# Optimization experiments

Hardware: AMD Instinct MI355X
Metric: run time of the kernel (lower is better)

Reference implementation:

```python
import jax, jax.numpy as jnp
import numpy as np

F8_MAX = 448.0  # max representable value of float8_e4m3fn


def setup_inputs() -> dict:
    key = jax.random.key(0)
    k1, k2, k3 = jax.random.split(key, 3)
    inp = jax.random.normal(k1, (4, 2048, 4096), dtype=jnp.float32)
    weight = jax.random.normal(k2, (4096, 16384), dtype=jnp.float32) * 0.02  # [in, out] (stored transposed)
    bias = jax.random.normal(k3, (16384,), dtype=jnp.float32)
    return {"inp": inp, "weight": weight, "bias": bias}


def reference(inp, weight, bias):
    # --- weight quantization (from_float with abs-max observer) ---
    w_scale = jnp.max(jnp.abs(weight)) / F8_MAX                      # scalar fp32
    w_q = (weight * (1.0 / w_scale)).astype(jnp.float8_e4m3fn)       # [in, out] fp8

    # --- dynamic input quantization: amax = max(|min|, |max|) ---
    x = inp.reshape(-1, inp.shape[-1])                               # [N, in]
    amax = jnp.maximum(jnp.abs(jnp.min(x)), jnp.abs(jnp.max(x)))
    x_scale = amax / F8_MAX
    x_q = (x * (1.0 / x_scale)).astype(jnp.float8_e4m3fn)            # [N, in] fp8

    # --- fp8_gemm_v2: dequant-matmul with fused scales + bias ---
    out = jnp.matmul(x_q.astype(jnp.float32), w_q.astype(jnp.float32))
    out = out * (x_scale * w_scale) + bias                           # [N, out]
    return out.reshape(inp.shape[:-1] + (weight.shape[1],))
```

## Files before the change

### kernel.cpp

```cpp
#include <hip/hip_runtime.h>
#include <stdint.h>
#include <stddef.h>

typedef float f32x16 __attribute__((ext_vector_type(16)));
typedef int i32x8 __attribute__((ext_vector_type(8)));

union Frag32 { long l[4]; i32x8 v; };


__global__ void absmax_kernel(const float4* __restrict__ x, size_t n4,
                              unsigned int* __restrict__ out) {
  size_t idx = (size_t)blockIdx.x * blockDim.x + threadIdx.x;
  size_t stride = (size_t)gridDim.x * blockDim.x;
  float m = 0.f;
  for (size_t i = idx; i < n4; i += stride) {
    float4 v = x[i];
    m = fmaxf(m, fmaxf(fmaxf(fabsf(v.x), fabsf(v.y)),
                       fmaxf(fabsf(v.z), fabsf(v.w))));
  }
#pragma unroll
  for (int off = 32; off > 0; off >>= 1)
    m = fmaxf(m, __shfl_xor(m, off));
  if ((threadIdx.x & 63) == 0)
    atomicMax(out, __float_as_uint(m));
}

__global__ void scales_kernel(float* __restrict__ s) {
  const unsigned int* u = (const unsigned int*)s;
  float wmax = __uint_as_float(u[0]);
  float xmax = __uint_as_float(u[1]);
  float w_scale = wmax / 448.0f;
  float x_scale = xmax / 448.0f;
  s[2] = 1.0f / w_scale;
  s[3] = 1.0f / x_scale;
  s[4] = x_scale * w_scale;
}

__global__ void quantize_x_kernel(const float4* __restrict__ x,
                                  uint8_t* __restrict__ xq,
                                  const float* __restrict__ scales,
                                  int K, int n_chunks) {
  const float inv = scales[3];
  const int kslots = K >> 5;
  int idx = blockIdx.x * blockDim.x + threadIdx.x;
  const int stride = gridDim.x * blockDim.x;
  for (; idx < n_chunks; idx += stride) {
    const int slot = idx >> 9;
    const int p16 = idx & 511;
    const int row = p16 >> 1;
    const int kkb0 = (p16 & 1) << 4;
    const int mblk = slot / kslots;
    const int ksl = slot - mblk * kslots;
    const size_t f4 = ((size_t)(mblk * 256 + row) * K + ksl * 32 + kkb0) >> 2;
    const float4 v0 = x[f4 + 0], v1 = x[f4 + 1], v2 = x[f4 + 2], v3 = x[f4 + 3];
    uint32_t c0 = __builtin_amdgcn_cvt_pk_fp8_f32(v0.x * inv, v0.y * inv, 0, false);
    c0 = __builtin_amdgcn_cvt_pk_fp8_f32(v0.z * inv, v0.w * inv, c0, true);
    uint32_t c1 = __builtin_amdgcn_cvt_pk_fp8_f32(v1.x * inv, v1.y * inv, 0, false);
    c1 = __builtin_amdgcn_cvt_pk_fp8_f32(v1.z * inv, v1.w * inv, c1, true);
    uint32_t c2 = __builtin_amdgcn_cvt_pk_fp8_f32(v2.x * inv, v2.y * inv, 0, false);
    c2 = __builtin_amdgcn_cvt_pk_fp8_f32(v2.z * inv, v2.w * inv, c2, true);
    uint32_t c3 = __builtin_amdgcn_cvt_pk_fp8_f32(v3.x * inv, v3.y * inv, 0, false);
    c3 = __builtin_amdgcn_cvt_pk_fp8_f32(v3.z * inv, v3.w * inv, c3, true);
    const unsigned long long L0 = (unsigned long long)c0 | ((unsigned long long)c1 << 32);
    const unsigned long long L1 = (unsigned long long)c2 | ((unsigned long long)c3 << 32);
    const int Lc = row * 32 + kkb0;
    const int mask = ((row >> 2) & 3) << 3;
    const int addr0 = Lc ^ (mask & 16);
    uint8_t* p = xq + (size_t)slot * 8192;
    *(unsigned long long*)(p + addr0 + (mask & 8)) = L0;
    *(unsigned long long*)(p + addr0 + (8 ^ (mask & 8))) = L1;
  }
}

__global__ void quantize_wT_kernel(const float* __restrict__ w,
                                   uint8_t* __restrict__ wqt,
                                   const float* __restrict__ scales,
                                   int N, int K) {
  __shared__ uint8_t tile[64][68];
  const float inv = scales[2];
  const int tn = blockIdx.x;
  const int tk = blockIdx.y;
  const int t = threadIdx.x;
  {
    const int rr = t >> 4;
    const int cc4 = t & 15;
#pragma unroll
    for (int i = 0; i < 4; ++i) {
      const int row = rr + i * 16;
      const float4 v = *(const float4*)&w[(size_t)(tk * 64 + row) * N + tn * 64 + cc4 * 4];
      uint32_t c = __builtin_amdgcn_cvt_pk_fp8_f32(v.x * inv, v.y * inv, 0, false);
      c = __builtin_amdgcn_cvt_pk_fp8_f32(v.z * inv, v.w * inv, c, true);
      *(uint32_t*)&tile[row][cc4 * 4] = c;
    }
  }
  __syncthreads();
  {
    const int nrow = t & 63;
    const int kc16 = t >> 6;
    unsigned long long L0 = 0, L1 = 0;
#pragma unroll
    for (int j = 0; j < 8; ++j)
      L0 |= (unsigned long long)tile[kc16 * 16 + j][nrow] << (8 * j);
#pragma unroll
    for (int j = 0; j < 8; ++j)
      L1 |= (unsigned long long)tile[kc16 * 16 + 8 + j][nrow] << (8 * j);
    const int n_g = tn * 64 + nrow;
    const int k0g = tk * 64 + kc16 * 16;
    const size_t slot = (size_t)(n_g >> 8) * (K >> 5) + (k0g >> 5);
    const int row = n_g & 255;
    const int kkb0 = k0g & 31;
    const int Lc = row * 32 + kkb0;
    const int mask = ((row >> 2) & 3) << 3;
    const int addr0 = Lc ^ (mask & 16);
    uint8_t* p = wqt + slot * 8192;
    *(unsigned long long*)(p + addr0 + (mask & 8)) = L0;
    *(unsigned long long*)(p + addr0 + (8 ^ (mask & 8))) = L1;
  }
}

#define T_BM 256
#define T_BN 256
#define UNIT_SCALE 0x7F7F7F7F

__device__ __forceinline__ void gl_lds16(const uint8_t* g, uint8_t* lds) {
  __builtin_amdgcn_global_load_lds(
      (const __attribute__((address_space(1))) void*)g,
      (__attribute__((address_space(3))) void*)lds, 16, 0, 0);
}

__global__ __launch_bounds__(1024, 4) void gemm_fp8_mx(
    const uint8_t* __restrict__ Aq, const uint8_t* __restrict__ BqT,
    const float* __restrict__ bias, const float* __restrict__ scales,
    float* __restrict__ C, int M, int N, int K) {
  extern __shared__ uint8_t smem[];
  uint8_t* const Ar = smem;
  uint8_t* const Br = smem + 65536;

  const int ntn = N / T_BN;
  const int bid = blockIdx.x;
  const int m0 = (bid / ntn) * T_BM;
  const int n0 = (bid % ntn) * T_BN;

  const int tid = threadIdx.x;
  const int w = tid >> 6;
  const int l = tid & 63;
  const int wr = w >> 2;
  const int wc = w & 3;

  const int kslots = K >> 5;

  const int soff = w * 1024 + l * 16;
  const uint8_t* a_src = Aq + (size_t)(m0 >> 8) * kslots * 8192 + soff;
  const uint8_t* b_src = BqT + (size_t)(n0 >> 8) * kslots * 8192 + soff;

  const int h = l >> 5;
  const int rl = l & 31;
  int aoff[2][4], boff[2][4];
#pragma unroll
  for (int mt = 0; mt < 2; ++mt) {
    const int ra = wr * 64 + mt * 32 + rl;
    const int rb = wc * 64 + mt * 32 + rl;
#pragma unroll
    for (int j = 0; j < 4; ++j) {
      aoff[mt][j] = h * 8192 + ra * 32 + ((j ^ ((ra >> 2) & 3)) * 8);
      boff[mt][j] = h * 8192 + rb * 32 + ((j ^ ((rb >> 2) & 3)) * 8);
    }
  }

  f32x16 acc[2][2];
#pragma unroll
  for (int i = 0; i < 2; ++i)
#pragma unroll
    for (int j = 0; j < 2; ++j) acc[i][j] = 0.f;

  const int NP = K >> 6;

  gl_lds16(a_src, Ar + soff);
  gl_lds16(b_src, Br + soff);
  gl_lds16(a_src + 16384, Ar + 16384 + soff);
  gl_lds16(b_src + 16384, Br + 16384 + soff);
  asm volatile("s_waitcnt vmcnt(2)" ::: "memory");
  __builtin_amdgcn_s_barrier();

  for (int p = 0; p < NP; ++p) {
    const int ss = (p + 2 < NP) ? (p + 2) : (p - 2);
    const int rslot = ((p + 2) & 3) * 16384;
    gl_lds16(a_src + (size_t)ss * 16384, Ar + rslot + soff);
    gl_lds16(b_src + (size_t)ss * 16384, Br + rslot + soff);

    const uint8_t* Asl = Ar + (p & 3) * 16384;
    const uint8_t* Bsl = Br + (p & 3) * 16384;
    Frag32 af[2], bf[2];
#pragma unroll
    for (int t2 = 0; t2 < 2; ++t2)
#pragma unroll
      for (int j = 0; j < 4; ++j) {
        af[t2].l[j] = *(const long*)(Asl + aoff[t2][j]);
        bf[t2].l[j] = *(const long*)(Bsl + boff[t2][j]);
      }

    __builtin_amdgcn_s_setprio(1);
    acc[0][0] = __builtin_amdgcn_mfma_scale_f32_32x32x64_f8f6f4(
        af[0].v, bf[0].v, acc[0][0], 0, 0, 0, UNIT_SCALE, 0, UNIT_SCALE);
    acc[1][0] = __builtin_amdgcn_mfma_scale_f32_32x32x64_f8f6f4(
        af[1].v, bf[0].v, acc[1][0], 0, 0, 0, UNIT_SCALE, 0, UNIT_SCALE);
    acc[0][1] = __builtin_amdgcn_mfma_scale_f32_32x32x64_f8f6f4(
        af[0].v, bf[1].v, acc[0][1], 0, 0, 0, UNIT_SCALE, 0, UNIT_SCALE);
    acc[1][1] = __builtin_amdgcn_mfma_scale_f32_32x32x64_f8f6f4(
        af[1].v, bf[1].v, acc[1][1], 0, 0, 0, UNIT_SCALE, 0, UNIT_SCALE);
    __builtin_amdgcn_s_setprio(0);

    asm volatile("s_waitcnt vmcnt(2)" ::: "memory");
    __builtin_amdgcn_s_barrier();
  }
  asm volatile("s_waitcnt vmcnt(0)" ::: "memory");

  const float s = scales[4];
  const int colb = n0 + wc * 64 + rl;
  const int rowb = m0 + wr * 64 + 4 * h;
#pragma unroll
  for (int nt = 0; nt < 2; ++nt) {
    const int col = colb + nt * 32;
    const float bv = bias[col];
#pragma unroll
    for (int mt = 0; mt < 2; ++mt) {
#pragma unroll
      for (int r = 0; r < 16; ++r) {
        const int row = rowb + mt * 32 + (r & 3) + 8 * (r >> 2);
        C[(size_t)row * N + col] = acc[mt][nt][r] * s + bv;
      }
    }
  }
}

extern "C" void kernel_launch(void* const* d_in, const int* in_sizes, int n_in,
                              void* d_out, int out_size, void* d_ws, size_t ws_size,
                              hipStream_t stream) {
  const float* inp = (const float*)d_in[0];
  const float* weight = (const float*)d_in[1];
  const float* bias = (const float*)d_in[2];
  float* out = (float*)d_out;

  const int N = in_sizes[2];
  const int K = in_sizes[1] / N;
  const int M = in_sizes[0] / K;

  uint8_t* ws = (uint8_t*)d_ws;
  float* scales = (float*)ws;
  uint8_t* xq = ws + 256;
  uint8_t* wqt = ws + 256 + (size_t)M * K;

  hipMemsetAsync(d_ws, 0, 256, stream);

  absmax_kernel<<<2048, 256, 0, stream>>>((const float4*)weight,
                                          (size_t)K * N / 4,
                                          (unsigned int*)ws + 0);
  absmax_kernel<<<2048, 256, 0, stream>>>((const float4*)inp,
                                          (size_t)M * K / 4,
                                          (unsigned int*)ws + 1);
  scales_kernel<<<1, 1, 0, stream>>>(scales);

  quantize_x_kernel<<<4096, 256, 0, stream>>>((const float4*)inp, xq, scales,
                                              K, M * K / 16);
  quantize_wT_kernel<<<dim3(N / 64, K / 64), 256, 0, stream>>>(weight, wqt,
                                                               scales, N, K);

  gemm_fp8_mx<<<(M / T_BM) * (N / T_BN), 1024, 131072, stream>>>(
      xq, wqt, bias, scales, out, M, N, K);
}
```

Before: 886.8 us.

## Enlarge per-wave GEMM tiles, rework weight transpose-quantize, drop scales kernel

The GEMM drops from 16 waves to 8 waves per block, and each wave now computes a 64x128 output tile with 8 MFMA accumulators instead of 4. This raises register-level reuse of A fragments and halves LDS fragment traffic per MFMA. The weight quantize kernel now transposes fp32 values through LDS, converts 32 consecutive k values per thread, and writes 16-byte stores instead of gathering bytes. The separate scales kernel is removed and each consumer computes its scale from the amax words, and absmax processes two float4 per iteration. The risks are higher register pressure and lower occupancy in the GEMM, plus a larger LDS tile in the transpose kernel.

```diff
diff --git a/kernel.cpp b/kernel.cpp
--- a/kernel.cpp
+++ b/kernel.cpp
@@ -10,14 +10,18 @@
 
 __global__ void absmax_kernel(const float4* __restrict__ x, size_t n4,
                               unsigned int* __restrict__ out) {
-  size_t idx = (size_t)blockIdx.x * blockDim.x + threadIdx.x;
-  size_t stride = (size_t)gridDim.x * blockDim.x;
-  float m = 0.f;
+  size_t idx = ((size_t)blockIdx.x * blockDim.x + threadIdx.x) * 2;
+  size_t stride = (size_t)gridDim.x * blockDim.x * 2;
+  float m0 = 0.f, m1 = 0.f;
   for (size_t i = idx; i < n4; i += stride) {
     float4 v = x[i];
-    m = fmaxf(m, fmaxf(fmaxf(fabsf(v.x), fabsf(v.y)),
-                       fmaxf(fabsf(v.z), fabsf(v.w))));
-  }
+    float4 u = x[i + 1];
+    m0 = fmaxf(m0, fmaxf(fmaxf(fabsf(v.x), fabsf(v.y)),
+                         fmaxf(fabsf(v.z), fabsf(v.w))));
+    m1 = fmaxf(m1, fmaxf(fmaxf(fabsf(u.x), fabsf(u.y)),
+                         fmaxf(fabsf(u.z), fabsf(u.w))));
+  }
+  float m = fmaxf(m0, m1);
 #pragma unroll
   for (int off = 32; off > 0; off >>= 1)
     m = fmaxf(m, __shfl_xor(m, off));
@@ -25,22 +29,12 @@
     atomicMax(out, __float_as_uint(m));
 }
 
-__global__ void scales_kernel(float* __restrict__ s) {
-  const unsigned int* u = (const unsigned int*)s;
-  float wmax = __uint_as_float(u[0]);
-  float xmax = __uint_as_float(u[1]);
-  float w_scale = wmax / 448.0f;
-  float x_scale = xmax / 448.0f;
-  s[2] = 1.0f / w_scale;
-  s[3] = 1.0f / x_scale;
-  s[4] = x_scale * w_scale;
-}
-
 __global__ void quantize_x_kernel(const float4* __restrict__ x,
                                   uint8_t* __restrict__ xq,
-                                  const float* __restrict__ scales,
+                                  const unsigned int* __restrict__ amax,
                                   int K, int n_chunks) {
-  const float inv = scales[3];
+  const float x_scale = __uint_as_float(amax[1]) / 448.0f;
+  const float inv = 1.0f / x_scale;
   const int kslots = K >> 5;
   int idx = blockIdx.x * blockDim.x + threadIdx.x;
   const int stride = gridDim.x * blockDim.x;
@@ -74,47 +68,54 @@
 
 __global__ void quantize_wT_kernel(const float* __restrict__ w,
                                    uint8_t* __restrict__ wqt,
-                                   const float* __restrict__ scales,
+                                   const unsigned int* __restrict__ amax,
                                    int N, int K) {
-  __shared__ uint8_t tile[64][68];
-  const float inv = scales[2];
+  __shared__ float tileF[64][129];
+  const float w_scale = __uint_as_float(amax[0]) / 448.0f;
+  const float inv = 1.0f / w_scale;
   const int tn = blockIdx.x;
   const int tk = blockIdx.y;
   const int t = threadIdx.x;
   {
-    const int rr = t >> 4;
-    const int cc4 = t & 15;
-#pragma unroll
-    for (int i = 0; i < 4; ++i) {
-      const int row = rr + i * 16;
-      const float4 v = *(const float4*)&w[(size_t)(tk * 64 + row) * N + tn * 64 + cc4 * 4];
-      uint32_t c = __builtin_amdgcn_cvt_pk_fp8_f32(v.x * inv, v.y * inv, 0, false);
-      c = __builtin_amdgcn_cvt_pk_fp8_f32(v.z * inv, v.w * inv, c, true);
-      *(uint32_t*)&tile[row][cc4 * 4] = c;
+    const int nn4 = t & 15;
+    const int kk0 = t >> 4;
+#pragma unroll
+    for (int i = 0; i < 8; ++i) {
+      const int kk = kk0 + i * 16;
+      const float4 v =
+          *(const float4*)&w[(size_t)(tk * 128 + kk) * N + tn * 64 + nn4 * 4];
+      tileF[nn4 * 4 + 0][kk] = v.x;
+      tileF[nn4 * 4 + 1][kk] = v.y;
+      tileF[nn4 * 4 + 2][kk] = v.z;
+      tileF[nn4 * 4 + 3][kk] = v.w;
     }
   }
   __syncthreads();
   {
-    const int nrow = t & 63;
-    const int kc16 = t >> 6;
-    unsigned long long L0 = 0, L1 = 0;
-#pragma unroll
-    for (int j = 0; j < 8; ++j)
-      L0 |= (unsigned long long)tile[kc16 * 16 + j][nrow] << (8 * j);
-#pragma unroll
-    for (int j = 0; j < 8; ++j)
-      L1 |= (unsigned long long)tile[kc16 * 16 + 8 + j][nrow] << (8 * j);
-    const int n_g = tn * 64 + nrow;
-    const int k0g = tk * 64 + kc16 * 16;
+    const int n = t & 63;
+    const int c = t >> 6;
+    unsigned long long q[4];
+#pragma unroll
+    for (int cc = 0; cc < 4; ++cc) {
+      const float4 u0 = *(const float4*)&tileF[n][c * 32 + cc * 8];
+      const float4 u1 = *(const float4*)&tileF[n][c * 32 + cc * 8 + 4];
+      uint32_t lo = __builtin_amdgcn_cvt_pk_fp8_f32(u0.x * inv, u0.y * inv, 0, false);
+      lo = __builtin_amdgcn_cvt_pk_fp8_f32(u0.z * inv, u0.w * inv, lo, true);
+      uint32_t hi = __builtin_amdgcn_cvt_pk_fp8_f32(u1.x * inv, u1.y * inv, 0, false);
+      hi = __builtin_amdgcn_cvt_pk_fp8_f32(u1.z * inv, u1.w * inv, hi, true);
+      q[cc] = (unsigned long long)lo | ((unsigned long long)hi << 32);
+    }
+    const int n_g = tn * 64 + n;
+    const int k0g = tk * 128 + c * 32;
     const size_t slot = (size_t)(n_g >> 8) * (K >> 5) + (k0g >> 5);
     const int row = n_g & 255;
-    const int kkb0 = k0g & 31;
-    const int Lc = row * 32 + kkb0;
-    const int mask = ((row >> 2) & 3) << 3;
-    const int addr0 = Lc ^ (mask & 16);
-    uint8_t* p = wqt + slot * 8192;
-    *(unsigned long long*)(p + addr0 + (mask & 8)) = L0;
-    *(unsigned long long*)(p + addr0 + (8 ^ (mask & 8))) = L1;
+    const int mask = (row >> 2) & 3;
+    ulonglong2 s0, s1;
+    s0.x = q[0 ^ mask]; s0.y = q[1 ^ mask];
+    s1.x = q[2 ^ mask]; s1.y = q[3 ^ mask];
+    uint8_t* pbase = wqt + slot * 8192 + row * 32;
+    *(ulonglong2*)(pbase) = s0;
+    *(ulonglong2*)(pbase + 16) = s1;
   }
 }
 
@@ -128,9 +129,9 @@
       (__attribute__((address_space(3))) void*)lds, 16, 0, 0);
 }
 
-__global__ __launch_bounds__(1024, 4) void gemm_fp8_mx(
+__global__ __launch_bounds__(512, 2) void gemm_fp8_mx(
     const uint8_t* __restrict__ Aq, const uint8_t* __restrict__ BqT,
-    const float* __restrict__ bias, const float* __restrict__ scales,
+    const float* __restrict__ bias, const unsigned int* __restrict__ amax,
     float* __restrict__ C, int M, int N, int K) {
   extern __shared__ uint8_t smem[];
   uint8_t* const Ar = smem;
@@ -144,82 +145,95 @@
   const int tid = threadIdx.x;
   const int w = tid >> 6;
   const int l = tid & 63;
-  const int wr = w >> 2;
-  const int wc = w & 3;
+  const int wr = w >> 1;
+  const int wc = w & 1;
 
   const int kslots = K >> 5;
 
-  const int soff = w * 1024 + l * 16;
+  const int soff = w * 2048 + l * 16;
   const uint8_t* a_src = Aq + (size_t)(m0 >> 8) * kslots * 8192 + soff;
   const uint8_t* b_src = BqT + (size_t)(n0 >> 8) * kslots * 8192 + soff;
 
   const int h = l >> 5;
   const int rl = l & 31;
-  int aoff[2][4], boff[2][4];
+  int aoff[2][4], boff[4][4];
 #pragma unroll
   for (int mt = 0; mt < 2; ++mt) {
     const int ra = wr * 64 + mt * 32 + rl;
-    const int rb = wc * 64 + mt * 32 + rl;
-#pragma unroll
-    for (int j = 0; j < 4; ++j) {
+#pragma unroll
+    for (int j = 0; j < 4; ++j)
       aoff[mt][j] = h * 8192 + ra * 32 + ((j ^ ((ra >> 2) & 3)) * 8);
-      boff[mt][j] = h * 8192 + rb * 32 + ((j ^ ((rb >> 2) & 3)) * 8);
-    }
-  }
-
-  f32x16 acc[2][2];
+  }
+#pragma unroll
+  for (int nt = 0; nt < 4; ++nt) {
+    const int rb = wc * 128 + nt * 32 + rl;
+#pragma unroll
+    for (int j = 0; j < 4; ++j)
+      boff[nt][j] = h * 8192 + rb * 32 + ((j ^ ((rb >> 2) & 3)) * 8);
+  }
+
+  f32x16 acc[2][4];
 #pragma unroll
   for (int i = 0; i < 2; ++i)
 #pragma unroll
-    for (int j = 0; j < 2; ++j) acc[i][j] = 0.f;
+    for (int j = 0; j < 4; ++j) acc[i][j] = 0.f;
 
   const int NP = K >> 6;
 
-  gl_lds16(a_src, Ar + soff);
-  gl_lds16(b_src, Br + soff);
-  gl_lds16(a_src + 16384, Ar + 16384 + soff);
-  gl_lds16(b_src + 16384, Br + 16384 + soff);
-  asm volatile("s_waitcnt vmcnt(2)" ::: "memory");
+#pragma unroll
+  for (int sidx = 0; sidx < 2; ++sidx) {
+    gl_lds16(a_src + sidx * 16384, Ar + sidx * 16384 + soff);
+    gl_lds16(a_src + sidx * 16384 + 1024, Ar + sidx * 16384 + soff + 1024);
+    gl_lds16(b_src + sidx * 16384, Br + sidx * 16384 + soff);
+    gl_lds16(b_src + sidx * 16384 + 1024, Br + sidx * 16384 + soff + 1024);
+  }
+  asm volatile("s_waitcnt vmcnt(4)" ::: "memory");
   __builtin_amdgcn_s_barrier();
 
   for (int p = 0; p < NP; ++p) {
     const int ss = (p + 2 < NP) ? (p + 2) : (p - 2);
     const int rslot = ((p + 2) & 3) * 16384;
     gl_lds16(a_src + (size_t)ss * 16384, Ar + rslot + soff);
+    gl_lds16(a_src + (size_t)ss * 16384 + 1024, Ar + rslot + soff + 1024);
     gl_lds16(b_src + (size_t)ss * 16384, Br + rslot + soff);
+    gl_lds16(b_src + (size_t)ss * 16384 + 1024, Br + rslot + soff + 1024);
 
     const uint8_t* Asl = Ar + (p & 3) * 16384;
     const uint8_t* Bsl = Br + (p & 3) * 16384;
-    Frag32 af[2], bf[2];
-#pragma unroll
-    for (int t2 = 0; t2 < 2; ++t2)
-#pragma unroll
-      for (int j = 0; j < 4; ++j) {
-        af[t2].l[j] = *(const long*)(Asl + aoff[t2][j]);
-        bf[t2].l[j] = *(const long*)(Bsl + boff[t2][j]);
-      }
+    Frag32 af[2], bf[4];
+#pragma unroll
+    for (int mt = 0; mt < 2; ++mt)
+#pragma unroll
+      for (int j = 0; j < 4; ++j)
+        af[mt].l[j] = *(const long*)(Asl + aoff[mt][j]);
+#pragma unroll
+    for (int nt = 0; nt < 4; ++nt)
+#pragma unroll
+      for (int j = 0; j < 4; ++j)
+        bf[nt].l[j] = *(const long*)(Bsl + boff[nt][j]);
 
     __builtin_amdgcn_s_setprio(1);
-    acc[0][0] = __builtin_amdgcn_mfma_scale_f32_32x32x64_f8f6f4(
-        af[0].v, bf[0].v, acc[0][0], 0, 0, 0, UNIT_SCALE, 0, UNIT_SCALE);
-    acc[1][0] = __builtin_amdgcn_mfma_scale_f32_32x32x64_f8f6f4(
-        af[1].v, bf[0].v, acc[1][0], 0, 0, 0, UNIT_SCALE, 0, UNIT_SCALE);
-    acc[0][1] = __builtin_amdgcn_mfma_scale_f32_32x32x64_f8f6f4(
-        af[0].v, bf[1].v, acc[0][1], 0, 0, 0, UNIT_SCALE, 0, UNIT_SCALE);
-    acc[1][1] = __builtin_amdgcn_mfma_scale_f32_32x32x64_f8f6f4(
-        af[1].v, bf[1].v, acc[1][1], 0, 0, 0, UNIT_SCALE, 0, UNIT_SCALE);
+#pragma unroll
+    for (int nt = 0; nt < 4; ++nt) {
+      acc[0][nt] = __builtin_amdgcn_mfma_scale_f32_32x32x64_f8f6f4(
+          af[0].v, bf[nt].v, acc[0][nt], 0, 0, 0, UNIT_SCALE, 0, UNIT_SCALE);
+      acc[1][nt] = __builtin_amdgcn_mfma_scale_f32_32x32x64_f8f6f4(
+          af[1].v, bf[nt].v, acc[1][nt], 0, 0, 0, UNIT_SCALE, 0, UNIT_SCALE);
+    }
     __builtin_amdgcn_s_setprio(0);
 
-    asm volatile("s_waitcnt vmcnt(2)" ::: "memory");
+    asm volatile("s_waitcnt vmcnt(4)" ::: "memory");
     __builtin_amdgcn_s_barrier();
   }
   asm volatile("s_waitcnt vmcnt(0)" ::: "memory");
 
-  const float s = scales[4];
-  const int colb = n0 + wc * 64 + rl;
+  const float x_scale = __uint_as_float(amax[1]) / 448.0f;
+  const float w_scale = __uint_as_float(amax[0]) / 448.0f;
+  const float s = x_scale * w_scale;
+  const int colb = n0 + wc * 128 + rl;
   const int rowb = m0 + wr * 64 + 4 * h;
 #pragma unroll
-  for (int nt = 0; nt < 2; ++nt) {
+  for (int nt = 0; nt < 4; ++nt) {
     const int col = colb + nt * 32;
     const float bv = bias[col];
 #pragma unroll
@@ -246,25 +260,22 @@
   const int M = in_sizes[0] / K;
 
   uint8_t* ws = (uint8_t*)d_ws;
-  float* scales = (float*)ws;
+  unsigned int* amax = (unsigned int*)ws;
   uint8_t* xq = ws + 256;
   uint8_t* wqt = ws + 256 + (size_t)M * K;
 
-  hipMemsetAsync(d_ws, 0, 256, stream);
+  hipMemsetAsync(d_ws, 0, 8, stream);
 
   absmax_kernel<<<2048, 256, 0, stream>>>((const float4*)weight,
-                                          (size_t)K * N / 4,
-                                          (unsigned int*)ws + 0);
+                                          (size_t)K * N / 4, amax + 0);
   absmax_kernel<<<2048, 256, 0, stream>>>((const float4*)inp,
-                                          (size_t)M * K / 4,
-                                          (unsigned int*)ws + 1);
-  scales_kernel<<<1, 1, 0, stream>>>(scales);
-
-  quantize_x_kernel<<<4096, 256, 0, stream>>>((const float4*)inp, xq, scales,
+                                          (size_t)M * K / 4, amax + 1);
+
+  quantize_x_kernel<<<4096, 256, 0, stream>>>((const float4*)inp, xq, amax,
                                               K, M * K / 16);
-  quantize_wT_kernel<<<dim3(N / 64, K / 64), 256, 0, stream>>>(weight, wqt,
-                                                               scales, N, K);
-
-  gemm_fp8_mx<<<(M / T_BM) * (N / T_BN), 1024, 131072, stream>>>(
-      xq, wqt, bias, scales, out, M, N, K);
-}
+  quantize_wT_kernel<<<dim3(N / 64, K / 128), 256, 0, stream>>>(weight, wqt,
+                                                                amax, N, K);
+
+  gemm_fp8_mx<<<(M / T_BM) * (N / T_BN), 512, 131072, stream>>>(
+      xq, wqt, bias, amax, out, M, N, K);
+}
```

New measurement: 900.3 us. Within noise of the previous version (+1.5%).
